# Kernel tuning notes

Measured on AMD Instinct MI355X. Metric: run time of the kernel, lower is better.

Reference implementation:

```python
import jax, jax.numpy as jnp
import numpy as np

B, S, E, H, D = 4, 2048, 1024, 16, 64


def setup_inputs() -> dict:
    key = jax.random.key(0)
    ks = jax.random.split(key, 6)
    scale_in = 1.0 / np.sqrt(E)
    return {
        "x": jax.random.normal(ks[0], (B, S, E), dtype=jnp.float32),
        "Wq": jax.random.normal(ks[1], (H, E, D), dtype=jnp.float32) * scale_in,
        "bq": jnp.zeros((H, D), dtype=jnp.float32),
        "Wk": jax.random.normal(ks[2], (H, E, D), dtype=jnp.float32) * scale_in,
        "bk": jnp.zeros((H, D), dtype=jnp.float32),
        "Wv": jax.random.normal(ks[3], (H, E, D), dtype=jnp.float32) * scale_in,
        "bv": jnp.zeros((H, D), dtype=jnp.float32),
        "Wo": jax.random.normal(ks[4], (H * D, E), dtype=jnp.float32) * (1.0 / np.sqrt(H * D)),
        "bo": jnp.zeros((E,), dtype=jnp.float32),
    }


def reference(x, Wq, bq, Wk, bk, Wv, bv, Wo, bo):
    # Per-head Q/K/V projections, batched over heads: [B,S,E] x [H,E,D] -> [B,H,S,D]
    q = jnp.einsum("bse,hed->bhsd", x, Wq) + bq[None, :, None, :]
    k = jnp.einsum("bse,hed->bhsd", x, Wk) + bk[None, :, None, :]
    v = jnp.einsum("bse,hed->bhsd", x, Wv) + bv[None, :, None, :]

    d = q.shape[-1]
    scores = jnp.einsum("bhqd,bhkd->bhqk", q, k) / jnp.sqrt(jnp.asarray(d, q.dtype))
    # Causal mask (registered tril buffer of size max_seq_len in HeadAttention)
    seq = scores.shape[-1]
    causal = jnp.tril(jnp.ones((seq, seq), dtype=bool))
    scores = jnp.where(causal[None, None, :, :], scores, jnp.asarray(-1e9, scores.dtype))
    attn = jax.nn.softmax(scores, axis=-1)
    out = jnp.einsum("bhqk,bhkd->bhqd", attn, v)  # [B,H,S,D]

    # Concat heads: [B,S,H*D], then output projection (dropout is identity in eval)
    out = out.transpose(0, 2, 1, 3).reshape(out.shape[0], out.shape[2], -1)
    return out @ Wo + bo
```

## Files before the change

kernel.cpp:

```cpp
#include <hip/hip_runtime.h>

typedef __bf16 bf16x8 __attribute__((ext_vector_type(8)));
typedef __bf16 bf16x4 __attribute__((ext_vector_type(4)));
typedef float  f32x4  __attribute__((ext_vector_type(4)));

#define B_    4
#define S_    2048
#define E_    1024
#define H_    16
#define D_    64
#define MROWS (B_*S_)

#define SCORE_SCALE 0.18033688011112043f

__device__ __forceinline__ void load_lds16(const void* g, void* l) {
  __builtin_amdgcn_global_load_lds((__attribute__((address_space(1))) void*)g,
                                   (__attribute__((address_space(3))) void*)l,
                                   16, 0, 0);
}

__device__ __forceinline__ f32x4 mfma16(bf16x8 a, bf16x8 b, f32x4 c) {
  return __builtin_amdgcn_mfma_f32_16x16x32_bf16(a, b, c, 0, 0, 0);
}

__device__ __forceinline__ int swz(int row, int dchunk) {
  return row * 64 + ((dchunk ^ (row & 7)) * 8);
}


__global__ void prep(const float4* __restrict__ x, const float* __restrict__ Wq,
                     const float* __restrict__ Wk, const float* __restrict__ Wv,
                     const float* __restrict__ bq, const float* __restrict__ bk,
                     const float* __restrict__ bv, const float* __restrict__ Wo,
                     __bf16* __restrict__ xb, __bf16* __restrict__ Wt,
                     float* __restrict__ bqkv, __bf16* __restrict__ Wot) {
  __shared__ float t[64][65];
  int bid = blockIdx.x;
  if (bid < 8192) {
    int id = bid * 256 + threadIdx.x;
    float4 v = x[id];
    bf16x4 o = { (__bf16)v.x, (__bf16)v.y, (__bf16)v.z, (__bf16)v.w };
    *(bf16x4*)(xb + 4 * (size_t)id) = o;
    return;
  }
  int tx = threadIdx.x & 63;
  int ty = threadIdx.x >> 6;
  if (bid < 8960) {
    int b2 = bid - 8192;
    int e0 = (b2 & 15) * 64;
    int h  = (b2 >> 4) & 15;
    int p  = b2 >> 8;
    const float* W    = (p == 0) ? Wq : (p == 1) ? Wk : Wv;
    const float* bsrc = (p == 0) ? bq : (p == 1) ? bk : bv;
#pragma unroll
    for (int r = 0; r < 16; ++r) {
      int eL = ty + r * 4;
      t[eL][tx] = W[((size_t)h * 1024 + (e0 + eL)) * 64 + tx];
    }
    __syncthreads();
#pragma unroll
    for (int r = 0; r < 16; ++r) {
      int d = ty + r * 4;
      Wt[((size_t)(p * 1024 + h * 64 + d)) * 1024 + e0 + tx] = (__bf16)t[tx][d];
    }
    if ((b2 & 15) == 0 && threadIdx.x < 64)
      bqkv[p * 1024 + h * 64 + threadIdx.x] = bsrc[h * 64 + threadIdx.x];
  } else {
    int b2 = bid - 8960;
    int hd0 = (b2 >> 4) * 64;
    int e0  = (b2 & 15) * 64;
#pragma unroll
    for (int r = 0; r < 16; ++r) {
      int hdL = ty + r * 4;
      t[hdL][tx] = Wo[(size_t)(hd0 + hdL) * 1024 + e0 + tx];
    }
    __syncthreads();
#pragma unroll
    for (int r = 0; r < 16; ++r) {
      int eL = ty + r * 4;
      Wot[(size_t)(e0 + eL) * 1024 + hd0 + tx] = (__bf16)t[tx][eL];
    }
  }
}


template <int MODE, int BN, int NDIM>
__global__ __launch_bounds__(512, 4) void gemm8h(const __bf16* __restrict__ A,
                                                 const __bf16* __restrict__ Bt,
                                                 const float* __restrict__ bias,
                                                 void* __restrict__ Cout,
                                                 __bf16* __restrict__ VT) {
  constexpr int K = 1024;
  constexpr int NB = BN / 64;
  constexpr int WC = BN / 4;
  __shared__ __attribute__((aligned(16))) __bf16 As[2 * 128 * 64];
  __shared__ __attribute__((aligned(16))) __bf16 Bs[2 * BN * 64];

  int tid = threadIdx.x, wave = tid >> 6, lane = tid & 63;
  int quad = lane >> 4, cc = lane & 15;
  constexpr int nb = NDIM / BN;
  int nwg = (int)gridDim.x;
  int bid = (int)blockIdx.x;
  bid = (bid & 7) * (nwg >> 3) + (bid >> 3);
  int bm = bid / nb, bn = bid % nb;
  const __bf16* Abase = A + (size_t)bm * 128 * K;
  const __bf16* Bbase = Bt + (size_t)bn * BN * K;
  int wrow = (wave >> 2) * 64;
  int wcol = (wave & 3) * WC;

  f32x4 acc[4][NB];
#pragma unroll
  for (int m = 0; m < 4; ++m)
#pragma unroll
    for (int n = 0; n < NB; ++n) acc[m][n] = (f32x4){0.f, 0.f, 0.f, 0.f};

  int srl = tid >> 3;
  int sch = tid & 7;
  int scol = (sch ^ (srl & 7)) * 8;

#define STAGE_A(t, sub, buf)                                                   \
  load_lds16(Abase + (size_t)((sub) * 64 + srl) * K + (t) * 64 + scol,         \
             &As[(buf) * 8192 + (sub) * 4096 + tid * 8])
#define STAGE_B(t, sub, buf)                                                   \
  load_lds16(Bbase + (size_t)((sub) * 64 + srl) * K + (t) * 64 + scol,         \
             &Bs[(buf) * (BN * 64) + (sub) * 4096 + tid * 8])

#pragma unroll
  for (int s = 0; s < 2; ++s) STAGE_A(0, s, 0);
#pragma unroll
  for (int s = 0; s < NB; ++s) STAGE_B(0, s, 0);
#pragma unroll
  for (int s = 0; s < 2; ++s) STAGE_A(1, s, 1);
  asm volatile("s_waitcnt vmcnt(2)" ::: "memory");
  __builtin_amdgcn_sched_barrier(0);
  asm volatile("s_barrier" ::: "memory");

  bf16x8 af[4][2], bfr[NB][2];

#define RD_B(buf)                                                              \
  _Pragma("unroll") for (int n = 0; n < NB; ++n)                               \
      _Pragma("unroll") for (int kk = 0; kk < 2; ++kk)                         \
          bfr[n][kk] = *(const bf16x8*)&Bs[(buf) * (BN * 64) +                 \
                                           swz(wcol + n * 16 + cc, kk * 4 + quad)]
#define RD_A2(buf, mlo)                                                        \
  _Pragma("unroll") for (int m = mlo; m < (mlo) + 2; ++m)                      \
      _Pragma("unroll") for (int kk = 0; kk < 2; ++kk)                         \
          af[m][kk] = *(const bf16x8*)&As[(buf) * 8192 +                       \
                                          swz(wrow + m * 16 + cc, kk * 4 + quad)]
#define MFMA_M(m)                                                              \
  do {                                                                         \
    __builtin_amdgcn_s_setprio(1);                                             \
    _Pragma("unroll") for (int n = 0; n < NB; ++n)                             \
        _Pragma("unroll") for (int kk = 0; kk < 2; ++kk)                       \
            acc[m][n] = mfma16(af[m][kk], bfr[n][kk], acc[m][n]);              \
    __builtin_amdgcn_s_setprio(0);                                             \
  } while (0)
#define LGKM0                                                                  \
  asm volatile("s_waitcnt lgkmcnt(0)" ::: "memory");                           \
  __builtin_amdgcn_sched_barrier(0)
#define VMC2                                                                   \
  asm volatile("s_waitcnt vmcnt(2)" ::: "memory");                             \
  __builtin_amdgcn_sched_barrier(0)
#define BAR asm volatile("s_barrier" ::: "memory")

#pragma unroll 1
  for (int it = 0; it < 8; ++it) {
    int b_t = 2 * it + 1;
    int c_t = (2 * it + 2) & 15;
    int d_t = (2 * it + 3) & 15;
    RD_B(0); RD_A2(0, 0);
    STAGE_B(b_t, 0, 1); STAGE_B(b_t, 1, 1);
    LGKM0; MFMA_M(0); BAR;
    RD_A2(0, 2);
    if (NB >= 3) STAGE_B(b_t, 2, 1);
    LGKM0; MFMA_M(1); BAR;
    STAGE_A(c_t, 0, 0); STAGE_A(c_t, 1, 0);
    MFMA_M(2); BAR;
    MFMA_M(3);
    VMC2; BAR;
    RD_B(1); RD_A2(1, 0);
    STAGE_B(c_t, 0, 0); STAGE_B(c_t, 1, 0);
    LGKM0; MFMA_M(0); BAR;
    RD_A2(1, 2);
    if (NB >= 3) STAGE_B(c_t, 2, 0);
    LGKM0; MFMA_M(1); BAR;
    STAGE_A(d_t, 0, 1); STAGE_A(d_t, 1, 1);
    MFMA_M(2); BAR;
    MFMA_M(3);
    VMC2; BAR;
  }
  asm volatile("s_waitcnt vmcnt(0)" ::: "memory");

#pragma unroll
  for (int n = 0; n < NB; ++n) {
    int gcol = bn * BN + wcol + n * 16 + cc;
    float bv = bias[gcol];
#pragma unroll
    for (int m = 0; m < 4; ++m) {
      int grow0 = bm * 128 + wrow + m * 16 + quad * 4;
      if (MODE == 0) {
#pragma unroll
        for (int r = 0; r < 4; ++r)
          ((float*)Cout)[(size_t)(grow0 + r) * NDIM + gcol] = acc[m][n][r] + bv;
      } else if (gcol < 2048) {
        float sc = (gcol < 1024) ? SCORE_SCALE : 1.0f;
#pragma unroll
        for (int r = 0; r < 4; ++r)
          ((__bf16*)Cout)[(size_t)(grow0 + r) * 2048 + gcol] =
              (__bf16)((acc[m][n][r] + bv) * sc);
      } else {
        int bh = (grow0 >> 11) * 16 + ((gcol >> 6) & 15);
        int d  = gcol & 63;
        bf16x4 pk;
#pragma unroll
        for (int r = 0; r < 4; ++r) pk[r] = (__bf16)(acc[m][n][r] + bv);
        *(bf16x4*)&VT[((size_t)(bh * 64 + d)) * 2048 + (grow0 & 2047)] = pk;
      }
    }
  }
#undef STAGE_A
#undef STAGE_B
#undef RD_B
#undef RD_A2
#undef MFMA_M
#undef LGKM0
#undef VMC2
#undef BAR
}


__global__ __launch_bounds__(256, 4) void attn(const __bf16* __restrict__ QKb,
                                               const __bf16* __restrict__ VT,
                                               __bf16* __restrict__ O) {
  int bx = blockIdx.x;
  int bh = bx & 63;
  int g  = bx >> 6;
  int qt = (g < 8) ? (15 - g) : (g - 8);
  int h  = bh & 15;
  int b  = bh >> 4;
  int q0 = qt * 128;
  int tid = threadIdx.x, wave = tid >> 6, lane = tid & 63;
  int quad = lane >> 4, c = lane & 15;

  __shared__ __attribute__((aligned(16))) __bf16 smem[20480];
  __bf16* Ps = smem + wave * 1024;
  __bf16* Ks = smem + 4096;
  __bf16* Vs = smem + 12288;

  const __bf16* Vbase = VT + (size_t)bh * (64 * 2048);
  int qwave = q0 + wave * 32;

  bf16x8 qf[2][2];
#pragma unroll
  for (int i = 0; i < 2; ++i)
#pragma unroll
    for (int kk = 0; kk < 2; ++kk)
      qf[i][kk] = *(const bf16x8*)&QKb[(size_t)(b * S_ + qwave + i * 16 + c) * 2048 +
                                       h * 64 + (kk * 4 + quad) * 8];

  {
    const __bf16* Kb = QKb + (size_t)(b * S_) * 2048 + 1024 + h * 64;
#pragma unroll
    for (int p = 0; p < 2; ++p) {
      int gi = tid + p * 256;
      int row = gi >> 3, pch = gi & 7;
      load_lds16(Kb + (size_t)row * 2048 + (pch ^ (row & 7)) * 8, &Ks[gi * 8]);
      load_lds16(Vbase + (size_t)row * 2048 + (pch ^ (row & 7)) * 8, &Vs[gi * 8]);
    }
  }
  __syncthreads();

  const __bf16 one_b = (__bf16)1.0f;
  bf16x8 ones = { one_b, one_b, one_b, one_b, one_b, one_b, one_b, one_b };

  f32x4 acc_o[2][4], acc_l[2];
#pragma unroll
  for (int i = 0; i < 2; ++i) {
    acc_l[i] = (f32x4){0.f, 0.f, 0.f, 0.f};
#pragma unroll
    for (int j = 0; j < 4; ++j) acc_o[i][j] = (f32x4){0.f, 0.f, 0.f, 0.f};
  }

  int ntiles = qt * 2 + 2;
  for (int t = 0; t < ntiles; ++t) {
    int cur = t & 1;
    if (t + 1 < ntiles) {
      int kv1 = (t + 1) * 64;
      const __bf16* Kb = QKb + (size_t)(b * S_ + kv1) * 2048 + 1024 + h * 64;
      const __bf16* Vb = Vbase + kv1;
#pragma unroll
      for (int p = 0; p < 2; ++p) {
        int gi = tid + p * 256;
        int row = gi >> 3, pch = gi & 7;
        load_lds16(Kb + (size_t)row * 2048 + (pch ^ (row & 7)) * 8,
                   &Ks[(cur ^ 1) * 4096 + gi * 8]);
        load_lds16(Vb + (size_t)row * 2048 + (pch ^ (row & 7)) * 8,
                   &Vs[(cur ^ 1) * 4096 + gi * 8]);
      }
      asm volatile("s_waitcnt vmcnt(4)" ::: "memory");
    } else {
      asm volatile("s_waitcnt vmcnt(0)" ::: "memory");
    }
    __builtin_amdgcn_sched_barrier(0);
    asm volatile("s_barrier" ::: "memory");

    int kv0 = t * 64;
    if (kv0 <= qwave + 31) {
      const __bf16* Kc = Ks + cur * 4096;
      const __bf16* Vc = Vs + cur * 4096;

      f32x4 acc_t[2][4];
#pragma unroll
      for (int i = 0; i < 2; ++i)
#pragma unroll
        for (int j = 0; j < 4; ++j) acc_t[i][j] = (f32x4){0.f, 0.f, 0.f, 0.f};
      bf16x8 kf[4][2];
#pragma unroll
      for (int j = 0; j < 4; ++j)
#pragma unroll
        for (int kk = 0; kk < 2; ++kk)
          kf[j][kk] = *(const bf16x8*)&Kc[swz(j * 16 + c, kk * 4 + quad)];
      __builtin_amdgcn_s_setprio(1);
#pragma unroll
      for (int i = 0; i < 2; ++i)
#pragma unroll
        for (int j = 0; j < 4; ++j)
#pragma unroll
          for (int kk = 0; kk < 2; ++kk)
            acc_t[i][j] = mfma16(kf[j][kk], qf[i][kk], acc_t[i][j]);
      __builtin_amdgcn_s_setprio(0);

      bool domask = (kv0 + 63 > qwave);
      bf16x8 pf[2][2];
#pragma unroll
      for (int i = 0; i < 2; ++i) {
        int q_g = qwave + i * 16 + c;
#pragma unroll
        for (int j = 0; j < 4; ++j) {
          bf16x4 pk;
#pragma unroll
          for (int r = 0; r < 4; ++r) {
            float p = __builtin_amdgcn_exp2f(acc_t[i][j][r]);
            if (domask) {
              int kv = kv0 + j * 16 + quad * 4 + r;
              p = (kv > q_g) ? 0.f : p;
            }
            pk[r] = (__bf16)p;
          }
          int dch8 = j * 2 + (quad >> 1);
          int phys = c * 64 + ((dch8 ^ (c & 7)) * 8) + (quad & 1) * 4;
          *(bf16x4*)&Ps[phys] = pk;
        }
#pragma unroll
        for (int kk = 0; kk < 2; ++kk)
          pf[i][kk] = *(const bf16x8*)&Ps[swz(c, kk * 4 + quad)];
      }

      bf16x8 vf[4][2];
#pragma unroll
      for (int j = 0; j < 4; ++j)
#pragma unroll
        for (int kk = 0; kk < 2; ++kk)
          vf[j][kk] = *(const bf16x8*)&Vc[swz(j * 16 + c, kk * 4 + quad)];
      __builtin_amdgcn_s_setprio(1);
#pragma unroll
      for (int i = 0; i < 2; ++i) {
#pragma unroll
        for (int j = 0; j < 4; ++j)
#pragma unroll
          for (int kk = 0; kk < 2; ++kk)
            acc_o[i][j] = mfma16(pf[i][kk], vf[j][kk], acc_o[i][j]);
        acc_l[i] = mfma16(pf[i][0], ones, acc_l[i]);
        acc_l[i] = mfma16(pf[i][1], ones, acc_l[i]);
      }
      __builtin_amdgcn_s_setprio(0);
    }

    asm volatile("s_barrier" ::: "memory");
  }

  __bf16* Obase = O + (size_t)(b * S_ + q0) * 1024 + h * 64;
#pragma unroll
  for (int i = 0; i < 2; ++i)
#pragma unroll
    for (int r = 0; r < 4; ++r) {
      float rl = 1.0f / acc_l[i][r];
      int row = wave * 32 + i * 16 + quad * 4 + r;
#pragma unroll
      for (int j = 0; j < 4; ++j)
        Obase[(size_t)row * 1024 + j * 16 + c] = (__bf16)(acc_o[i][j][r] * rl);
    }
}


extern "C" void kernel_launch(void* const* d_in, const int* in_sizes, int n_in,
                              void* d_out, int out_size, void* d_ws, size_t ws_size,
                              hipStream_t stream) {
  (void)in_sizes; (void)n_in; (void)out_size; (void)ws_size;
  const float* x  = (const float*)d_in[0];
  const float* Wq = (const float*)d_in[1];
  const float* bq = (const float*)d_in[2];
  const float* Wk = (const float*)d_in[3];
  const float* bk = (const float*)d_in[4];
  const float* Wv = (const float*)d_in[5];
  const float* bv = (const float*)d_in[6];
  const float* Wo = (const float*)d_in[7];
  const float* bo = (const float*)d_in[8];

  char* w = (char*)d_ws;
  __bf16* xb   = (__bf16*)(w);
  __bf16* Wt   = (__bf16*)(w + (16ull << 20));
  __bf16* Wot  = (__bf16*)(w + (22ull << 20));
  float*  bqkv = (float*) (w + (24ull << 20));
  __bf16* QKb  = (__bf16*)(w + (25ull << 20));
  __bf16* Ob   = (__bf16*)(w + (57ull << 20));
  __bf16* VT   = (__bf16*)(w + (73ull << 20));

  prep<<<9216, 256, 0, stream>>>((const float4*)x, Wq, Wk, Wv, bq, bk, bv, Wo,
                                 xb, Wt, bqkv, Wot);
  gemm8h<1, 192, 3072><<<1024, 512, 0, stream>>>(xb, Wt, bqkv, (void*)QKb, VT);
  attn<<<1024, 256, 0, stream>>>(QKb, VT, Ob);
  gemm8h<0, 128, 1024><<<512, 512, 0, stream>>>(Ob, Wot, bo, d_out, nullptr);
}
```

Before: 234.6 us.

## Replace QKV projection GEMM with 256x256-tile ping-pong scheduled kernel

Adds a new QKV projection GEMM kernel that uses 256x256 output tiles per 512-thread workgroup, with 384 workgroups and an XCD-aware block remap. The K loop is hand-scheduled: quarter-tile async global-to-LDS loads are interleaved with MFMA groups, using explicit barriers, waitcnts and setprio to overlap memory and compute. The aim is more operand reuse per LDS load and less global traffic than the earlier 128x192 tiles. In exchange, the kernel uses 64 KB of LDS and many accumulator registers, so occupancy drops to one workgroup per CU, and the hand-placed waits must be exactly right for correctness.

```diff
diff --git a/kernel.cpp b/kernel.cpp
--- a/kernel.cpp
+++ b/kernel.cpp
@@ -81,6 +81,150 @@
       Wot[(size_t)(e0 + eL) * 1024 + hd0 + tx] = (__bf16)t[tx][eL];
     }
   }
+}
+
+
+__global__ __launch_bounds__(512, 1) void gemm8t(const __bf16* __restrict__ A,
+                                                 const __bf16* __restrict__ Bt,
+                                                 const float* __restrict__ bias,
+                                                 __bf16* __restrict__ QKb,
+                                                 __bf16* __restrict__ VT) {
+  constexpr int K = 1024;
+  __shared__ __attribute__((aligned(16))) __bf16 As[2 * 16384];
+  __shared__ __attribute__((aligned(16))) __bf16 Bs[2 * 16384];
+
+  int tid = threadIdx.x, wave = tid >> 6, lane = tid & 63;
+  int quad = lane >> 4, cc = lane & 15;
+  int nwg = (int)gridDim.x;
+  int bid = (int)blockIdx.x;
+  bid = (bid & 7) * (nwg >> 3) + (bid >> 3);
+  int bm = bid / 12, bn = bid % 12;
+  const __bf16* Abase = A + (size_t)bm * 256 * K;
+  const __bf16* Bbase = Bt + (size_t)bn * 256 * K;
+  int wrow = (wave >> 2) * 128;
+  int wcol = (wave & 3) * 64;
+
+  f32x4 acc[8][4];
+#pragma unroll
+  for (int m = 0; m < 8; ++m)
+#pragma unroll
+    for (int n = 0; n < 4; ++n) acc[m][n] = (f32x4){0.f, 0.f, 0.f, 0.f};
+
+  int srl = tid >> 3;
+  int sch = tid & 7;
+  int scol = (sch ^ (srl & 7)) * 8;
+
+#define STAGE_A(t, q, buf)                                                     \
+  load_lds16(Abase + (size_t)((q) * 64 + srl) * K + (t) * 64 + scol,           \
+             &As[(buf) * 16384 + (q) * 4096 + tid * 8])
+#define STAGE_B(t, q, buf)                                                     \
+  load_lds16(Bbase + (size_t)((q) * 64 + srl) * K + (t) * 64 + scol,           \
+             &Bs[(buf) * 16384 + (q) * 4096 + tid * 8])
+
+#pragma unroll
+  for (int q = 0; q < 4; ++q) STAGE_A(0, q, 0);
+#pragma unroll
+  for (int q = 0; q < 4; ++q) STAGE_B(0, q, 0);
+#pragma unroll
+  for (int q = 0; q < 4; ++q) STAGE_B(1, q, 1);
+  asm volatile("s_waitcnt vmcnt(4)" ::: "memory");
+  __builtin_amdgcn_sched_barrier(0);
+  asm volatile("s_barrier" ::: "memory");
+
+  bf16x8 af[4][2], bfr[4][2];
+
+#define RD_A4(buf, mlo)                                                        \
+  _Pragma("unroll") for (int m2 = 0; m2 < 4; ++m2)                             \
+      _Pragma("unroll") for (int kk = 0; kk < 2; ++kk)                         \
+          af[m2][kk] = *(const bf16x8*)&As[(buf) * 16384 +                     \
+              swz(wrow + ((mlo) + m2) * 16 + cc, kk * 4 + quad)]
+#define RD_B2(buf, nlo)                                                        \
+  _Pragma("unroll") for (int n2 = 0; n2 < 2; ++n2)                             \
+      _Pragma("unroll") for (int kk = 0; kk < 2; ++kk)                         \
+          bfr[(nlo) + n2][kk] = *(const bf16x8*)&Bs[(buf) * 16384 +            \
+              swz(wcol + ((nlo) + n2) * 16 + cc, kk * 4 + quad)]
+#define MFMA_Q(mlo, nlo)                                                       \
+  do {                                                                         \
+    __builtin_amdgcn_s_setprio(1);                                             \
+    _Pragma("unroll") for (int m2 = 0; m2 < 4; ++m2)                           \
+        _Pragma("unroll") for (int n2 = 0; n2 < 2; ++n2)                       \
+            _Pragma("unroll") for (int kk = 0; kk < 2; ++kk)                   \
+                acc[(mlo) + m2][(nlo) + n2] =                                  \
+                    mfma16(af[m2][kk], bfr[(nlo) + n2][kk],                    \
+                           acc[(mlo) + m2][(nlo) + n2]);                       \
+    __builtin_amdgcn_s_setprio(0);                                             \
+  } while (0)
+#define LGKM0                                                                  \
+  asm volatile("s_waitcnt lgkmcnt(0)" ::: "memory");                           \
+  __builtin_amdgcn_sched_barrier(0)
+#define VMC4                                                                   \
+  asm volatile("s_waitcnt vmcnt(4)" ::: "memory");                             \
+  __builtin_amdgcn_sched_barrier(0)
+#define BAR asm volatile("s_barrier" ::: "memory")
+
+#pragma unroll 1
+  for (int it = 0; it < 8; ++it) {
+    int b1 = 2 * it + 1;
+    int c_t = (2 * it + 2) & 15;
+    int d_t = (2 * it + 3) & 15;
+    RD_A4(0, 0); RD_B2(0, 0);
+    STAGE_A(b1, 0, 1); STAGE_A(b1, 1, 1);
+    BAR; LGKM0; MFMA_Q(0, 0); BAR;
+    RD_B2(0, 2);
+    STAGE_A(b1, 2, 1); STAGE_A(b1, 3, 1);
+    BAR; LGKM0; MFMA_Q(0, 2); BAR;
+    RD_A4(0, 4);
+    STAGE_B(c_t, 0, 0); STAGE_B(c_t, 1, 0);
+    BAR; LGKM0; MFMA_Q(4, 0); BAR;
+    STAGE_B(c_t, 2, 0); STAGE_B(c_t, 3, 0);
+    BAR; MFMA_Q(4, 2);
+    VMC4; BAR;
+    RD_A4(1, 0); RD_B2(1, 0);
+    STAGE_A(c_t, 0, 0); STAGE_A(c_t, 1, 0);
+    BAR; LGKM0; MFMA_Q(0, 0); BAR;
+    RD_B2(1, 2);
+    STAGE_A(c_t, 2, 0); STAGE_A(c_t, 3, 0);
+    BAR; LGKM0; MFMA_Q(0, 2); BAR;
+    RD_A4(1, 4);
+    STAGE_B(d_t, 0, 1); STAGE_B(d_t, 1, 1);
+    BAR; LGKM0; MFMA_Q(4, 0); BAR;
+    STAGE_B(d_t, 2, 1); STAGE_B(d_t, 3, 1);
+    BAR; MFMA_Q(4, 2);
+    VMC4; BAR;
+  }
+  asm volatile("s_waitcnt vmcnt(0)" ::: "memory");
+
+#pragma unroll
+  for (int n = 0; n < 4; ++n) {
+    int gcol = bn * 256 + wcol + n * 16 + cc;
+    float bv = bias[gcol];
+#pragma unroll
+    for (int m = 0; m < 8; ++m) {
+      int grow0 = bm * 256 + wrow + m * 16 + quad * 4;
+      if (gcol < 2048) {
+        float sc = (gcol < 1024) ? SCORE_SCALE : 1.0f;
+#pragma unroll
+        for (int r = 0; r < 4; ++r)
+          QKb[(size_t)(grow0 + r) * 2048 + gcol] =
+              (__bf16)((acc[m][n][r] + bv) * sc);
+      } else {
+        int bh = (grow0 >> 11) * 16 + ((gcol >> 6) & 15);
+        int d  = gcol & 63;
+        bf16x4 pk;
+#pragma unroll
+        for (int r = 0; r < 4; ++r) pk[r] = (__bf16)(acc[m][n][r] + bv);
+        *(bf16x4*)&VT[((size_t)(bh * 64 + d)) * 2048 + (grow0 & 2047)] = pk;
+      }
+    }
+  }
+#undef STAGE_A
+#undef STAGE_B
+#undef RD_A4
+#undef RD_B2
+#undef MFMA_Q
+#undef LGKM0
+#undef VMC4
+#undef BAR
 }
 
 
@@ -418,7 +562,7 @@
 
   prep<<<9216, 256, 0, stream>>>((const float4*)x, Wq, Wk, Wv, bq, bk, bv, Wo,
                                  xb, Wt, bqkv, Wot);
-  gemm8h<1, 192, 3072><<<1024, 512, 0, stream>>>(xb, Wt, bqkv, (void*)QKb, VT);
+  gemm8t<<<384, 512, 0, stream>>>(xb, Wt, bqkv, QKb, VT);
   attn<<<1024, 256, 0, stream>>>(QKb, VT, Ob);
   gemm8h<0, 128, 1024><<<512, 512, 0, stream>>>(Ob, Wot, bo, d_out, nullptr);
 }
```

Result: slower. 253.4 us (+8.0%).
